# Kernel optimization log

Hardware: AMD Instinct MI355X
Metric: run time of the kernel (lower is better)

## Reference

```python
import jax, jax.numpy as jnp
import numpy as np

N_NODES = 50000
N_EDGES = 400000
D_IN = 512
D_OUT = 512


def setup_inputs() -> dict:
    key = jax.random.key(0)
    k1, k2, k3, k4, k5 = jax.random.split(key, 5)
    x = jax.random.normal(k1, (N_NODES, D_IN), dtype=jnp.float32)
    adj_rows = jax.random.randint(k2, (N_EDGES,), 0, N_NODES, dtype=jnp.int32)
    adj_cols = jax.random.randint(k3, (N_EDGES,), 0, N_NODES, dtype=jnp.int32)
    adj_vals = jax.random.uniform(k4, (N_EDGES,), dtype=jnp.float32)
    # Xavier uniform init for weight, zeros for bias (as in reset_parameters)
    limit = float(np.sqrt(6.0 / (D_IN + D_OUT)))
    weight = jax.random.uniform(k5, (D_IN, D_OUT), minval=-limit, maxval=limit, dtype=jnp.float32)
    bias = jnp.zeros((D_OUT,), dtype=jnp.float32)
    return {"x": x, "adj_rows": adj_rows, "adj_cols": adj_cols,
            "adj_vals": adj_vals, "weight": weight, "bias": bias}


def reference(x, adj_rows, adj_cols, adj_vals, weight, bias):
    # support = x @ W  : dense GEMM [N, D_in] x [D_in, D_out]
    support = jnp.matmul(x, weight)
    # output = spmm(adj, support): COO sparse-dense matmul via gather + segment_sum
    messages = adj_vals[:, None] * support[adj_cols]  # [E, D_out]
    output = jax.ops.segment_sum(messages, adj_rows, num_segments=N_NODES)
    return output + bias
```

## Files before the change

### kernel.cpp

```cpp
#include <hip/hip_runtime.h>

#define N_NODES 50000
#define N_EDGES 400000
#define DIM 512
#define NPAD 50048
#define MTILES 391
#define NTILES 4
#define NWG (MTILES * NTILES)

#define PREP_XBLK 12512
#define PREP_WBLK 1024
#define PREP_HBLK 1563

typedef short  short8  __attribute__((ext_vector_type(8)));
typedef unsigned short ushort8 __attribute__((ext_vector_type(8)));
typedef float  f32x4   __attribute__((ext_vector_type(4)));
typedef int    int2v   __attribute__((ext_vector_type(2)));

typedef __attribute__((address_space(1))) const unsigned short gu16;
typedef __attribute__((address_space(3))) unsigned short lu16;

__device__ __forceinline__ unsigned short f2bf(float f) {
    unsigned int u = __float_as_uint(f);
    u += 0x7fffu + ((u >> 16) & 1u);
    return (unsigned short)(u >> 16);
}
__device__ __forceinline__ float bf2f(unsigned short h) {
    return __uint_as_float(((unsigned int)h) << 16);
}

__global__ __launch_bounds__(256) void prep_kernel(const float* __restrict__ x,
                                                   unsigned short* __restrict__ xb,
                                                   const float* __restrict__ w,
                                                   unsigned short* __restrict__ wt,
                                                   const int* __restrict__ rows,
                                                   int* __restrict__ counts) {
    int b = blockIdx.x;
    if (b < PREP_XBLK) {
        size_t t = (size_t)b * 256 + threadIdx.x;
        size_t base = t * 8;
        int row = (int)(base >> 9);
        ushort8 o;
        if (row < N_NODES) {
            f32x4 a = *(const f32x4*)(x + base);
            f32x4 c = *(const f32x4*)(x + base + 4);
            o[0] = f2bf(a[0]); o[1] = f2bf(a[1]); o[2] = f2bf(a[2]); o[3] = f2bf(a[3]);
            o[4] = f2bf(c[0]); o[5] = f2bf(c[1]); o[6] = f2bf(c[2]); o[7] = f2bf(c[3]);
        } else {
            #pragma unroll
            for (int q = 0; q < 8; ++q) o[q] = 0;
        }
        *(ushort8*)(xb + base) = o;
    } else if (b < PREP_XBLK + PREP_WBLK) {
        int t = (b - PREP_XBLK) * 256 + threadIdx.x;
        int n = t >> 9, k = t & 511;
        wt[t] = f2bf(w[k * 512 + n]);
    } else {
        int e = (b - PREP_XBLK - PREP_WBLK) * 256 + threadIdx.x;
        if (e < N_EDGES) atomicAdd(&counts[rows[e]], 1);
    }
}

__global__ __launch_bounds__(512) void scan_blocks_kernel(const int* __restrict__ counts,
                                                          int* __restrict__ tmp,
                                                          int* __restrict__ partials) {
    __shared__ int sm[512];
    int i = blockIdx.x * 512 + threadIdx.x;
    int v = (i < N_NODES) ? counts[i] : 0;
    sm[threadIdx.x] = v;
    __syncthreads();
    #pragma unroll
    for (int off = 1; off < 512; off <<= 1) {
        int val = 0;
        if ((int)threadIdx.x >= off) val = sm[threadIdx.x - off];
        __syncthreads();
        if ((int)threadIdx.x >= off) sm[threadIdx.x] += val;
        __syncthreads();
    }
    if (i < N_NODES) tmp[i] = sm[threadIdx.x] - v;
    if (threadIdx.x == 511) partials[blockIdx.x] = sm[511];
}

__global__ __launch_bounds__(256) void add_offsets_kernel(const int* __restrict__ tmp,
                                                          const int* __restrict__ partials,
                                                          int* __restrict__ row_start,
                                                          int* __restrict__ cursor) {
    __shared__ int pin[128], pinc[128];
    const int tid = threadIdx.x;
    const int nb = 98;
    if (tid < 128) {
        int v = (tid < nb) ? partials[tid] : 0;
        pin[tid] = v;
        pinc[tid] = v;
    }
    __syncthreads();
    #pragma unroll
    for (int off = 1; off < 128; off <<= 1) {
        int val = 0;
        if (tid < 128 && tid >= off) val = pinc[tid - off];
        __syncthreads();
        if (tid < 128 && tid >= off) pinc[tid] += val;
        __syncthreads();
    }
    int i = blockIdx.x * 256 + tid;
    if (i < N_NODES) {
        int b9 = i >> 9;
        int excl = pinc[b9] - pin[b9];
        int rs = tmp[i] + excl;
        row_start[i] = rs;
        cursor[i] = rs;
    }
}

__global__ __launch_bounds__(256) void scatter_kernel(const int* __restrict__ rows,
                                                      const int* __restrict__ cols,
                                                      const float* __restrict__ vals,
                                                      int* __restrict__ cursor,
                                                      int2v* __restrict__ csr_cv) {
    int e = blockIdx.x * 256 + threadIdx.x;
    if (e < N_EDGES) {
        int r = rows[e];
        int p = atomicAdd(&cursor[r], 1);
        int2v cv;
        cv[0] = cols[e];
        cv[1] = __float_as_int(vals[e]);
        csr_cv[p] = cv;
    }
}

__global__ __launch_bounds__(256) void gemm_kernel(const unsigned short* __restrict__ Xb,
                                                   const unsigned short* __restrict__ Wt,
                                                   unsigned short* __restrict__ S) {
    __shared__ __align__(16) unsigned short As[128 * 64];
    __shared__ __align__(16) unsigned short Bs[128 * 64];

    const int q = NWG / 8, r8 = NWG % 8;
    int b = blockIdx.x;
    int xcd = b & 7, loc = b >> 3;
    int l = (xcd < r8 ? xcd * (q + 1) : r8 * (q + 1) + (xcd - r8) * q) + loc;
    const int m0 = (l >> 2) * 128;
    const int n0 = (l & 3) * 128;

    const int t = threadIdx.x;
    const int lane = t & 63;
    const int w = t >> 6;
    const int wr = w >> 1, wc = w & 1;
    const int fr = lane & 15;
    const int kg = lane >> 4;

    f32x4 acc[4][4];
    #pragma unroll
    for (int i = 0; i < 4; ++i)
        #pragma unroll
        for (int j = 0; j < 4; ++j)
            #pragma unroll
            for (int qq = 0; qq < 4; ++qq) acc[i][j][qq] = 0.0f;

    const int srow = w * 8 + (lane >> 3);
    const int scol = (lane & 7) * 8;
    const unsigned short* gA = Xb + (size_t)(m0 + srow) * DIM + scol;
    const unsigned short* gB = Wt + (size_t)(n0 + srow) * DIM + scol;
    lu16* AsW = (lu16*)As + w * 512;
    lu16* BsW = (lu16*)Bs + w * 512;

    for (int kk = 0; kk < DIM; kk += 64) {
        #pragma unroll
        for (int c = 0; c < 4; ++c) {
            __builtin_amdgcn_global_load_lds((gu16*)(gA + (size_t)c * 32 * DIM + kk), AsW + c * 2048, 16, 0, 0);
            __builtin_amdgcn_global_load_lds((gu16*)(gB + (size_t)c * 32 * DIM + kk), BsW + c * 2048, 16, 0, 0);
        }
        __syncthreads();

        short8 af[4][2], bf[4][2];
        #pragma unroll
        for (int mi = 0; mi < 4; ++mi)
            #pragma unroll
            for (int ks = 0; ks < 2; ++ks)
                af[mi][ks] = *(const short8*)&As[(wr * 64 + mi * 16 + fr) * 64 + ks * 32 + kg * 8];
        #pragma unroll
        for (int ni = 0; ni < 4; ++ni)
            #pragma unroll
            for (int ks = 0; ks < 2; ++ks)
                bf[ni][ks] = *(const short8*)&Bs[(wc * 64 + ni * 16 + fr) * 64 + ks * 32 + kg * 8];

        #pragma unroll
        for (int ks = 0; ks < 2; ++ks)
            #pragma unroll
            for (int mi = 0; mi < 4; ++mi)
                #pragma unroll
                for (int ni = 0; ni < 4; ++ni)
                    acc[mi][ni] = __builtin_amdgcn_mfma_f32_16x16x32_bf16(af[mi][ks], bf[ni][ks], acc[mi][ni], 0, 0, 0);

        __syncthreads();
    }

    #pragma unroll
    for (int mi = 0; mi < 4; ++mi) {
        #pragma unroll
        for (int ni = 0; ni < 4; ++ni) {
            int gr = m0 + wr * 64 + mi * 16 + kg * 4;
            int gc = n0 + wc * 64 + ni * 16 + fr;
            #pragma unroll
            for (int j = 0; j < 4; ++j)
                S[(size_t)(gr + j) * DIM + gc] = f2bf(acc[mi][ni][j]);
        }
    }
}

__global__ __launch_bounds__(256) void spmm_kernel(const unsigned short* __restrict__ S,
                                                   const int* __restrict__ row_start,
                                                   const int* __restrict__ counts,
                                                   const int2v* __restrict__ cv,
                                                   const float* __restrict__ bias,
                                                   float* __restrict__ out) {
    const int r = blockIdx.x * 4 + (threadIdx.x >> 6);
    const int lane = threadIdx.x & 63;
    const int s = row_start[r];
    const int n = counts[r];
    const size_t lo = (size_t)lane * 8;

    float acc[8];
    #pragma unroll
    for (int q = 0; q < 8; ++q) acc[q] = 0.0f;

    for (int j = 0; j < n; j += 8) {
        int   cc[8];
        float vv[8];
        #pragma unroll
        for (int k = 0; k < 8; ++k) {
            int2v e = cv[s + j + k];
            bool ok = (j + k < n);
            cc[k] = ok ? e[0] : 0;
            vv[k] = ok ? __int_as_float(e[1]) : 0.0f;
        }
        ushort8 xv[8];
        #pragma unroll
        for (int k = 0; k < 8; ++k)
            xv[k] = *(const ushort8*)&S[(size_t)cc[k] * DIM + lo];
        #pragma unroll
        for (int k = 0; k < 8; ++k)
            #pragma unroll
            for (int q = 0; q < 8; ++q)
                acc[q] += vv[k] * bf2f(xv[k][q]);
    }

    #pragma unroll
    for (int q = 0; q < 8; ++q) acc[q] += bias[lane * 8 + q];

    f32x4 o0, o1;
    #pragma unroll
    for (int q = 0; q < 4; ++q) { o0[q] = acc[q]; o1[q] = acc[4 + q]; }
    *(f32x4*)&out[(size_t)r * DIM + lo] = o0;
    *(f32x4*)&out[(size_t)r * DIM + lo + 4] = o1;
}

extern "C" void kernel_launch(void* const* d_in, const int* in_sizes, int n_in,
                              void* d_out, int out_size, void* d_ws, size_t ws_size,
                              hipStream_t stream) {
    const float* x    = (const float*)d_in[0];
    const int*   rows = (const int*)d_in[1];
    const int*   cols = (const int*)d_in[2];
    const float* vals = (const float*)d_in[3];
    const float* w    = (const float*)d_in[4];
    const float* bias = (const float*)d_in[5];
    float* out = (float*)d_out;

    char* ws = (char*)d_ws;
    size_t off = 0;
    auto alloc = [&](size_t bytes) -> char* {
        char* p = ws + off;
        off = (off + bytes + 255) & ~(size_t)255;
        return p;
    };
    unsigned short* Xb      = (unsigned short*)alloc((size_t)NPAD * DIM * 2);
    unsigned short* Wt      = (unsigned short*)alloc((size_t)DIM * DIM * 2);
    unsigned short* S       = (unsigned short*)alloc((size_t)NPAD * DIM * 2);
    int*            counts  = (int*)alloc((size_t)N_NODES * 4);
    int*            tmp     = (int*)alloc((size_t)N_NODES * 4);
    int*            rstart  = (int*)alloc((size_t)N_NODES * 4);
    int*            cursor  = (int*)alloc((size_t)N_NODES * 4);
    int*            partials= (int*)alloc(512);
    int2v*          csr_cv  = (int2v*)alloc((size_t)(N_EDGES + 8) * 8);

    hipMemsetAsync(counts, 0, (size_t)N_NODES * 4, stream);

    prep_kernel<<<PREP_XBLK + PREP_WBLK + PREP_HBLK, 256, 0, stream>>>(x, Xb, w, Wt, rows, counts);
    scan_blocks_kernel<<<98, 512, 0, stream>>>(counts, tmp, partials);
    add_offsets_kernel<<<(N_NODES + 255) / 256, 256, 0, stream>>>(tmp, partials, rstart, cursor);
    scatter_kernel<<<(N_EDGES + 255) / 256, 256, 0, stream>>>(rows, cols, vals, cursor, csr_cv);

    gemm_kernel<<<NWG, 256, 0, stream>>>(Xb, Wt, S);
    spmm_kernel<<<N_NODES / 4, 256, 0, stream>>>(S, rstart, counts, csr_cv, bias, out);
}
```

Measured before the change: 340.3 us.

## Fuse COO scatter into GEMM launch and shrink SpMM gather batch to four

New measurement: 335.1 us. About the same (-1.5%).

```diff
diff --git a/kernel.cpp b/kernel.cpp
--- a/kernel.cpp
+++ b/kernel.cpp
@@ -7,6 +7,7 @@
 #define MTILES 391
 #define NTILES 4
 #define NWG (MTILES * NTILES)
+#define SCAT_BLK 1563
 
 #define PREP_XBLK 12512
 #define PREP_WBLK 1024
@@ -112,30 +113,32 @@
     }
 }
 
-__global__ __launch_bounds__(256) void scatter_kernel(const int* __restrict__ rows,
-                                                      const int* __restrict__ cols,
-                                                      const float* __restrict__ vals,
-                                                      int* __restrict__ cursor,
-                                                      int2v* __restrict__ csr_cv) {
-    int e = blockIdx.x * 256 + threadIdx.x;
-    if (e < N_EDGES) {
-        int r = rows[e];
-        int p = atomicAdd(&cursor[r], 1);
-        int2v cv;
-        cv[0] = cols[e];
-        cv[1] = __float_as_int(vals[e]);
-        csr_cv[p] = cv;
-    }
-}
-
-__global__ __launch_bounds__(256) void gemm_kernel(const unsigned short* __restrict__ Xb,
-                                                   const unsigned short* __restrict__ Wt,
-                                                   unsigned short* __restrict__ S) {
+__global__ __launch_bounds__(256) void gemm_scatter_kernel(const unsigned short* __restrict__ Xb,
+                                                           const unsigned short* __restrict__ Wt,
+                                                           unsigned short* __restrict__ S,
+                                                           const int* __restrict__ rows,
+                                                           const int* __restrict__ cols,
+                                                           const float* __restrict__ vals,
+                                                           int* __restrict__ cursor,
+                                                           int2v* __restrict__ csr_cv) {
+    if (blockIdx.x < SCAT_BLK) {
+        int e = blockIdx.x * 256 + threadIdx.x;
+        if (e < N_EDGES) {
+            int r = rows[e];
+            int p = atomicAdd(&cursor[r], 1);
+            int2v cv;
+            cv[0] = cols[e];
+            cv[1] = __float_as_int(vals[e]);
+            csr_cv[p] = cv;
+        }
+        return;
+    }
+
     __shared__ __align__(16) unsigned short As[128 * 64];
     __shared__ __align__(16) unsigned short Bs[128 * 64];
 
     const int q = NWG / 8, r8 = NWG % 8;
-    int b = blockIdx.x;
+    int b = blockIdx.x - SCAT_BLK;
     int xcd = b & 7, loc = b >> 3;
     int l = (xcd < r8 ? xcd * (q + 1) : r8 * (q + 1) + (xcd - r8) * q) + loc;
     const int m0 = (l >> 2) * 128;
@@ -223,25 +226,30 @@
     #pragma unroll
     for (int q = 0; q < 8; ++q) acc[q] = 0.0f;
 
-    for (int j = 0; j < n; j += 8) {
-        int   cc[8];
-        float vv[8];
-        #pragma unroll
-        for (int k = 0; k < 8; ++k) {
-            int2v e = cv[s + j + k];
-            bool ok = (j + k < n);
-            cc[k] = ok ? e[0] : 0;
-            vv[k] = ok ? __int_as_float(e[1]) : 0.0f;
-        }
-        ushort8 xv[8];
-        #pragma unroll
-        for (int k = 0; k < 8; ++k)
-            xv[k] = *(const ushort8*)&S[(size_t)cc[k] * DIM + lo];
-        #pragma unroll
-        for (int k = 0; k < 8; ++k)
-            #pragma unroll
-            for (int q = 0; q < 8; ++q)
-                acc[q] += vv[k] * bf2f(xv[k][q]);
+    for (int j = 0; j < n; j += 4) {
+        int2v e0 = cv[s + j];
+        int2v e1 = cv[s + j + 1];
+        int2v e2 = cv[s + j + 2];
+        int2v e3 = cv[s + j + 3];
+        int c0 = e0[0];
+        int c1 = (j + 1 < n) ? e1[0] : 0;
+        int c2 = (j + 2 < n) ? e2[0] : 0;
+        int c3 = (j + 3 < n) ? e3[0] : 0;
+        float v0 = __int_as_float(e0[1]);
+        float v1 = (j + 1 < n) ? __int_as_float(e1[1]) : 0.0f;
+        float v2 = (j + 2 < n) ? __int_as_float(e2[1]) : 0.0f;
+        float v3 = (j + 3 < n) ? __int_as_float(e3[1]) : 0.0f;
+        ushort8 x0 = *(const ushort8*)&S[(size_t)c0 * DIM + lo];
+        ushort8 x1 = *(const ushort8*)&S[(size_t)c1 * DIM + lo];
+        ushort8 x2 = *(const ushort8*)&S[(size_t)c2 * DIM + lo];
+        ushort8 x3 = *(const ushort8*)&S[(size_t)c3 * DIM + lo];
+        #pragma unroll
+        for (int q = 0; q < 8; ++q) {
+            acc[q] += v0 * bf2f(x0[q]);
+            acc[q] += v1 * bf2f(x1[q]);
+            acc[q] += v2 * bf2f(x2[q]);
+            acc[q] += v3 * bf2f(x3[q]);
+        }
     }
 
     #pragma unroll
@@ -287,8 +295,8 @@
     prep_kernel<<<PREP_XBLK + PREP_WBLK + PREP_HBLK, 256, 0, stream>>>(x, Xb, w, Wt, rows, counts);
     scan_blocks_kernel<<<98, 512, 0, stream>>>(counts, tmp, partials);
     add_offsets_kernel<<<(N_NODES + 255) / 256, 256, 0, stream>>>(tmp, partials, rstart, cursor);
-    scatter_kernel<<<(N_EDGES + 255) / 256, 256, 0, stream>>>(rows, cols, vals, cursor, csr_cv);
-
-    gemm_kernel<<<NWG, 256, 0, stream>>>(Xb, Wt, S);
+
+    gemm_scatter_kernel<<<SCAT_BLK + NWG, 256, 0, stream>>>(Xb, Wt, S,
+                                                            rows, cols, vals, cursor, csr_cv);
     spmm_kernel<<<N_NODES / 4, 256, 0, stream>>>(S, rstart, counts, csr_cv, bias, out);
 }
```
